# Kernel optimization log

Measured on AMD Instinct MI355X. Metric: run time of the kernel, lower is better.

Reference implementation:

```python
import jax, jax.numpy as jnp
import numpy as np

PS = 8          # patch_size
NF = 16         # n_feats
B, H, W = 4, 256, 256
C = NF * PS * PS          # channel_num = 1024
INNER = 3 * C             # heads * channel_num (no head split in source)
SCALE = C ** -0.5         # heads_feats = channel_num
EPS = 1e-5


def _patch(x, shift):
    # reflect-pad then non-overlapping unfold (kernel=PS, stride=PS)
    s = PS // 4
    p = shift * s
    x = jnp.pad(x, ((0, 0), (0, 0), (p, PS - p), (p, PS - p)), mode='reflect')
    b, c, hp, wp = x.shape
    x = x.reshape(b, c, hp // PS, PS, wp // PS, PS)
    # F.unfold ordering: (c, kh, kw) flattened per patch, patches row-major
    x = x.transpose(0, 2, 4, 1, 3, 5).reshape(b, (hp // PS) * (wp // PS), c * PS * PS)
    return x  # [B, N, C*PS*PS]


def _unpatch(x, h, w):
    # inverse of non-overlapping unfold, then crop right/bottom by PS
    b, n, d = x.shape
    c = d // (PS * PS)
    nh, nw = (h + PS) // PS, (w + PS) // PS
    x = x.reshape(b, nh, nw, c, PS, PS).transpose(0, 3, 1, 4, 2, 5)
    x = x.reshape(b, c, nh * PS, nw * PS)
    return x[:, :, :h, :w]


def _ln(x, g, b):
    m = x.mean(-1, keepdims=True)
    v = ((x - m) ** 2).mean(-1, keepdims=True)
    return (x - m) / jnp.sqrt(v + EPS) * g + b


def setup_inputs():
    key = jax.random.key(0)
    ks = jax.random.split(key, 16)
    w = lambda k, shp: jax.random.normal(k, shp, jnp.float32) * 0.02
    return {
        'dr_img': jax.random.normal(ks[0], (B, NF, H, W), jnp.float32),
        'dr_ref': jax.random.normal(ks[1], (B, NF, H, W), jnp.float32),
        'cl_ref': jax.random.normal(ks[2], (B, NF, H, W), jnp.float32),
        'ln_g': jnp.ones((C,), jnp.float32), 'ln_b': jnp.zeros((C,), jnp.float32),
        'Wq': w(ks[3], (C, INNER)), 'bq': jnp.zeros((INNER,), jnp.float32),
        'Wk': w(ks[4], (C, INNER)), 'bk': jnp.zeros((INNER,), jnp.float32),
        'Wv': w(ks[5], (C, INNER)), 'bv': jnp.zeros((INNER,), jnp.float32),
        'Wo': w(ks[6], (INNER, C)), 'bo': jnp.zeros((C,), jnp.float32),
        'ff_ln_g': jnp.ones((C,), jnp.float32), 'ff_ln_b': jnp.zeros((C,), jnp.float32),
        'W1': w(ks[7], (C, C)), 'b1': jnp.zeros((C,), jnp.float32),
        'W2': w(ks[8], (C, C)), 'b2': jnp.zeros((C,), jnp.float32),
    }


def reference(dr_img, dr_ref, cl_ref, ln_g, ln_b, Wq, bq, Wk, bk, Wv, bv,
              Wo, bo, ff_ln_g, ff_ln_b, W1, b1, W2, b2):
    def attn(q, k, v):
        qp = _ln(q, ln_g, ln_b) @ Wq + bq          # [B,N,3C]
        kp = _ln(k, ln_g, ln_b) @ Wk + bk
        vp = _ln(v, ln_g, ln_b) @ Wv + bv
        a = jax.nn.softmax(jnp.einsum('bnd,bmd->bnm', qp, kp) * SCALE, axis=-1)
        return jnp.einsum('bnm,bmd->bnd', a, vp) @ Wo + bo

    def ff(x):
        h = _ln(x, ff_ln_g, ff_ln_b)
        return jax.nn.gelu(h @ W1 + b1, approximate=False) @ W2 + b2

    x = _patch(dr_img, 0)                           # [B,N,C]
    for shift in range(4):
        k = jax.lax.stop_gradient(_patch(dr_ref, shift))
        v = jax.lax.stop_gradient(_patch(cl_ref, shift))
        x = attn(x, k, v) + x
        x = ff(x) + x
    return _unpatch(x, H, W)
```

## Files before the change

### kernel.cpp

```cpp
#include <hip/hip_runtime.h>

typedef unsigned short u16;
typedef float f32x4 __attribute__((ext_vector_type(4)));
typedef __bf16 bf16v8 __attribute__((ext_vector_type(8)));
typedef u16 u16x4 __attribute__((ext_vector_type(4)));

#define WAITV(n) asm volatile("s_waitcnt vmcnt(" #n ")" ::: "memory")
#define BAR() asm volatile("s_barrier" ::: "memory")
#define LGKM0() do { asm volatile("s_waitcnt lgkmcnt(0)" ::: "memory"); \
                     __builtin_amdgcn_sched_barrier(0); } while (0)

__device__ __forceinline__ u16 f2bf(float f) {
  union { float f; unsigned int u; } v; v.f = f;
  unsigned int x = v.u;
  x += 0x7fffu + ((x >> 16) & 1u);
  return (u16)(x >> 16);
}

__device__ __forceinline__ int refl(int i, int n) {
  i = (i < 0) ? -i : i;
  return (i >= n) ? (2 * n - 2 - i) : i;
}

__device__ __forceinline__ void gload_lds16(const void* g, void* l) {
  __builtin_amdgcn_global_load_lds(
      (const __attribute__((address_space(1))) void*)g,
      (__attribute__((address_space(3))) void*)l, 16, 0, 0);
}

enum { EPI_BF16_BIAS = 0, EPI_F32 = 1, EPI_BF16 = 2, EPI_F32_RES = 3, EPI_GELU = 4,
       EPI_BF16_BIASROW = 5 };

__device__ __forceinline__ void xcd_remap(int& bx, int& by, int& bz) {
  const int gx = gridDim.x, gy = gridDim.y;
  const int nwg = gx * gy * (int)gridDim.z;
  const int orig = ((int)blockIdx.z * gy + (int)blockIdx.y) * gx + (int)blockIdx.x;
  const int q = nwg >> 3, r = nwg & 7;
  const int xcd = orig & 7, loc = orig >> 3;
  const int swz = (xcd < r ? xcd * (q + 1) : r * (q + 1) + (xcd - r) * q) + loc;
  const int gxy = gx * gy;
  bz = swz / gxy;
  const int rem = swz - bz * gxy;
  by = rem / gx; bx = rem - by * gx;
}

template <int EPI>
__global__ __launch_bounds__(512, 2) void gemm256(
    const u16* __restrict__ A, const u16* __restrict__ Bt, void* __restrict__ Cp,
    const float* __restrict__ bias, int K, int Nld, long sA, long sB, long sC, long sBias)
{
  extern __shared__ __align__(16) u16 smem[];

  const int t = threadIdx.x;
  int bx, by, bz; xcd_remap(bx, by, bz);
  const int m0 = by * 256, n0 = bx * 256;

  const long Kb = (long)K * 2;
  const int sr8 = t >> 3;
  const int schunk = ((t & 7) ^ (sr8 & 7)) * 16;
  const char* Ag = (const char*)(A + (long)bz * sA + (long)m0 * K) + (long)sr8 * Kb + schunk;
  const char* Bg = (const char*)(Bt + (long)bz * sB + (long)n0 * K) + (long)sr8 * Kb + schunk;

  auto SA = [&](int d, int kt, int i0, int i1) {
    const long ko = (long)kt * 128;
    gload_lds16(Ag + (long)i0 * 64 * Kb + ko, &smem[d * 32768 + i0 * 4096 + t * 8]);
    gload_lds16(Ag + (long)i1 * 64 * Kb + ko, &smem[d * 32768 + i1 * 4096 + t * 8]);
  };
  auto SB = [&](int d, int kt, int i0, int i1) {
    const long ko = (long)kt * 128;
    gload_lds16(Bg + (long)i0 * 64 * Kb + ko, &smem[d * 32768 + 16384 + i0 * 4096 + t * 8]);
    gload_lds16(Bg + (long)i1 * 64 * Kb + ko, &smem[d * 32768 + 16384 + i1 * 4096 + t * 8]);
  };

  const int w = t >> 6, lane = t & 63;
  const int wm = (w >> 2) * 128, wn = (w & 3) * 64;
  const int lr = lane & 15, hi = lane >> 4;
  const int rc0 = ((0 * 4 + hi) ^ (lr & 7)) * 8;
  const int rc1 = ((1 * 4 + hi) ^ (lr & 7)) * 8;

  f32x4 acc[8][4];
  const f32x4 vzero = {0.f, 0.f, 0.f, 0.f};
#pragma unroll
  for (int i = 0; i < 8; i++)
#pragma unroll
    for (int j = 0; j < 4; j++) acc[i][j] = vzero;

  const int NT = K >> 6, NI = NT >> 1;

  SA(0, 0, 0, 1); SA(0, 0, 2, 3); SB(0, 0, 0, 1); SB(0, 0, 2, 3);
  SB(1, 1, 0, 2); SB(1, 1, 1, 3); SA(1, 1, 0, 2);
  WAITV(6);
  BAR();

  for (int i = 0; i < NI; i++) {
    const int t0 = 2 * i;
    const bool last = (i == NI - 1);
#pragma unroll
    for (int h = 0; h < 2; h++) {
      const u16* Ad = &smem[h * 32768];
      const u16* Bd = Ad + 16384;
      bf16v8 b8[4][2];
#pragma unroll
      for (int q = 0; q < 4; q++) {
        bf16v8 a8[2][2];
#pragma unroll
        for (int j = 0; j < 2; j++) {
          const int rbase = (wm + (2 * q + j) * 16 + lr) * 64;
          a8[j][0] = *(const bf16v8*)&Ad[rbase + rc0];
          a8[j][1] = *(const bf16v8*)&Ad[rbase + rc1];
        }
        if (q == 0) {
#pragma unroll
          for (int ni = 0; ni < 4; ni++) {
            const int rbase = (wn + ni * 16 + lr) * 64;
            b8[ni][0] = *(const bf16v8*)&Bd[rbase + rc0];
            b8[ni][1] = *(const bf16v8*)&Bd[rbase + rc1];
          }
        }
        if (h == 0) {
          if (q == 0)           SA(1, t0 + 1, 1, 3);
          else if (!last) {
            if (q == 1)         SB(0, t0 + 2, 0, 2);
            else if (q == 2)    SB(0, t0 + 2, 1, 3);
            else                SA(0, t0 + 2, 0, 2);
          }
        } else if (!last) {
          if (q == 0)           SA(0, t0 + 2, 1, 3);
          else if (q == 1)      SB(1, t0 + 3, 0, 2);
          else if (q == 2)      SB(1, t0 + 3, 1, 3);
          else                  SA(1, t0 + 3, 0, 2);
        }
        BAR();
        LGKM0();
        __builtin_amdgcn_s_setprio(1);
#pragma unroll
        for (int j = 0; j < 2; j++)
#pragma unroll
          for (int ni = 0; ni < 4; ni++) {
            acc[2 * q + j][ni] = __builtin_amdgcn_mfma_f32_16x16x32_bf16(a8[j][0], b8[ni][0], acc[2 * q + j][ni], 0, 0, 0);
            acc[2 * q + j][ni] = __builtin_amdgcn_mfma_f32_16x16x32_bf16(a8[j][1], b8[ni][1], acc[2 * q + j][ni], 0, 0, 0);
          }
        __builtin_amdgcn_s_setprio(0);
        if (h == 0 && q == 3) { if (last) { WAITV(0); } else { WAITV(6); } }
        if (h == 1 && q == 3 && !last) { WAITV(6); }
        BAR();
      }
    }
  }

#pragma unroll
  for (int mi = 0; mi < 8; mi++) {
    const int r0 = m0 + wm + mi * 16 + hi * 4;
#pragma unroll
    for (int ni = 0; ni < 4; ni++) {
      const int col = n0 + wn + ni * 16 + lr;
      float bvv = 0.f;
      if constexpr (EPI == EPI_BF16_BIAS) bvv = bias[bz * sBias + col];
#pragma unroll
      for (int j = 0; j < 4; j++) {
        const long idx = (long)(r0 + j) * Nld + col;
        float val = acc[mi][ni][j] + bvv;
        if constexpr (EPI == EPI_BF16_BIASROW) val += bias[r0 + j];
        if constexpr (EPI == EPI_BF16_BIAS || EPI == EPI_BF16 || EPI == EPI_BF16_BIASROW) {
          ((u16*)Cp + (long)bz * sC)[idx] = f2bf(val);
        } else {
          ((float*)Cp + (long)bz * sC)[idx] = val;
        }
      }
    }
  }
}

template <int EPI>
__global__ __launch_bounds__(256, 2) void gemm128(
    const u16* __restrict__ A, const u16* __restrict__ Bt, void* __restrict__ Cp,
    const float* __restrict__ bias, int K, int ldb, int Nld, long sA, long sB, long sC)
{
  extern __shared__ __align__(16) u16 smem[];
  u16* As = smem;
  u16* Bs = smem + 16384;

  const int t = threadIdx.x;
  int bx, by, bz; xcd_remap(bx, by, bz);
  const int m0 = by * 128, n0 = bx * 128;

  const long Ka = (long)K * 2;
  const long Kbb = (long)ldb * 2;
  const int sc = ((t & 7) * 16) ^ (((t >> 3) & 7) << 4);
  const char* Ag = (const char*)(A + (long)bz * sA + (long)m0 * K) + (long)(t >> 3) * Ka + sc;
  const char* Bg = (const char*)(Bt + (long)bz * sB + (long)n0 * ldb) + (long)(t >> 3) * Kbb + sc;

  auto STAGE = [&](int d, int kt) {
    const long ko = (long)kt * 128;
#pragma unroll
    for (int i = 0; i < 4; i++)
      gload_lds16(Ag + (long)i * 32 * Ka + ko, &As[d * 8192 + i * 2048 + t * 8]);
#pragma unroll
    for (int i = 0; i < 4; i++)
      gload_lds16(Bg + (long)i * 32 * Kbb + ko, &Bs[d * 8192 + i * 2048 + t * 8]);
  };

  const int w = t >> 6, lane = t & 63;
  const int wm = (w >> 1) * 64, wn = (w & 1) * 64;
  const int lr = lane & 15, hi = lane >> 4;
  const int cx = (lr & 7) << 4;

  f32x4 acc[4][4];
  const f32x4 vzero = {0.f, 0.f, 0.f, 0.f};
#pragma unroll
  for (int i = 0; i < 4; i++)
#pragma unroll
    for (int j = 0; j < 4; j++) acc[i][j] = vzero;

  const int NT = K >> 6;
  STAGE(0, 0);
  STAGE(1, 1);

  for (int kt = 0; kt < NT; kt++) {
    const int d = kt & 1;
    if (kt + 1 < NT) { WAITV(8); } else { WAITV(0); }
    BAR();

    const u16* Ad = &As[d * 8192];
    const u16* Bd = &Bs[d * 8192];
#pragma unroll
    for (int ks = 0; ks < 2; ks++) {
      bf16v8 a8[4], b8[4];
      const int cb = ks * 64;
#pragma unroll
      for (int mi = 0; mi < 4; mi++)
        a8[mi] = *(const bf16v8*)&Ad[(wm + mi * 16 + lr) * 64 + (((cb + hi * 16) ^ cx) >> 1)];
#pragma unroll
      for (int ni = 0; ni < 4; ni++)
        b8[ni] = *(const bf16v8*)&Bd[(wn + ni * 16 + lr) * 64 + (((cb + hi * 16) ^ cx) >> 1)];
      __builtin_amdgcn_s_setprio(1);
#pragma unroll
      for (int mi = 0; mi < 4; mi++)
#pragma unroll
        for (int ni = 0; ni < 4; ni++)
          acc[mi][ni] = __builtin_amdgcn_mfma_f32_16x16x32_bf16(a8[mi], b8[ni], acc[mi][ni], 0, 0, 0);
      __builtin_amdgcn_s_setprio(0);
    }
    asm volatile("s_waitcnt lgkmcnt(0)\n\ts_barrier" ::: "memory");
    if (kt + 2 < NT) STAGE(d, kt + 2);
  }

#pragma unroll
  for (int mi = 0; mi < 4; mi++) {
    const int r0 = m0 + wm + mi * 16 + hi * 4;
#pragma unroll
    for (int ni = 0; ni < 4; ni++) {
      const int col = n0 + wn + ni * 16 + lr;
      float bvv = 0.f;
      if constexpr (EPI == EPI_F32_RES || EPI == EPI_GELU) bvv = bias[col];
#pragma unroll
      for (int j = 0; j < 4; j++) {
        const long idx = (long)(r0 + j) * Nld + col;
        const float val = acc[mi][ni][j] + bvv;
        if constexpr (EPI == EPI_F32) {
          ((float*)Cp + (long)bz * sC)[idx] = val;
        } else if constexpr (EPI == EPI_F32_RES) {
          ((float*)Cp + (long)bz * sC)[idx] += val;
        } else if constexpr (EPI == EPI_GELU) {
          const float gv = 0.5f * val * (1.f + erff(val * 0.70710678118654752440f));
          ((u16*)Cp + (long)bz * sC)[idx] = f2bf(gv);
        } else {
          ((u16*)Cp + (long)bz * sC)[idx] = f2bf(val);
        }
      }
    }
  }
}

__global__ __launch_bounds__(256) void ln_kernel(const float* __restrict__ X,
    const float* __restrict__ g, const float* __restrict__ be, u16* __restrict__ Y)
{
  const long row = blockIdx.x;
  const int t = threadIdx.x;
  const float* xr = X + row * 1024;
  f32x4 v = *(const f32x4*)&xr[t * 4];
  float s = v[0] + v[1] + v[2] + v[3];
  float q = v[0]*v[0] + v[1]*v[1] + v[2]*v[2] + v[3]*v[3];
#pragma unroll
  for (int off = 32; off; off >>= 1) { s += __shfl_xor(s, off); q += __shfl_xor(q, off); }
  __shared__ float red[8];
  if ((t & 63) == 0) { red[t >> 6] = s; red[4 + (t >> 6)] = q; }
  __syncthreads();
  s = red[0] + red[1] + red[2] + red[3];
  q = red[4] + red[5] + red[6] + red[7];
  const float mean = s * (1.f / 1024.f);
  const float rstd = rsqrtf(q * (1.f / 1024.f) - mean * mean + 1e-5f);
  f32x4 gv = *(const f32x4*)&g[t * 4];
  f32x4 bv = *(const f32x4*)&be[t * 4];
  u16x4 o;
#pragma unroll
  for (int i = 0; i < 4; i++) o[i] = f2bf((v[i] - mean) * rstd * gv[i] + bv[i]);
  *(u16x4*)&Y[row * 1024 + t * 4] = o;
}

__global__ __launch_bounds__(256) void patch_kernel(const float* __restrict__ img,
    float* __restrict__ X, int shift)
{
  const int n = blockIdx.x, b = blockIdx.y, t = threadIdx.x;
  float* xr = X + ((long)b * 1152 + n) * 1024;
  if (n >= 1089) {
    const f32x4 z = {0.f, 0.f, 0.f, 0.f};
    *(f32x4*)&xr[t * 4] = z;
    return;
  }
  const int p = shift * 2;
  const int ph = n / 33, pw = n - ph * 33;
  const int d0 = t * 4;
  const int c = d0 >> 6, kh = (d0 >> 3) & 7, kw0 = d0 & 7;
  const int hh = refl(ph * 8 + kh - p, 256);
  const float* src = img + ((long)(b * 16 + c) * 256 + hh) * 256;
  f32x4 v;
#pragma unroll
  for (int i = 0; i < 4; i++) v[i] = src[refl(pw * 8 + kw0 + i - p, 256)];
  *(f32x4*)&xr[d0] = v;
}

__global__ __launch_bounds__(256) void patch_ln_kernel(const float* __restrict__ img,
    const float* __restrict__ g, const float* __restrict__ be, u16* __restrict__ Y, int shift)
{
  const int n = blockIdx.x, b = blockIdx.y, t = threadIdx.x;
  u16* yr = Y + ((long)b * 1152 + n) * 1024;
  if (n >= 1089) {
    const u16x4 z = {0, 0, 0, 0};
    *(u16x4*)&yr[t * 4] = z;
    return;
  }
  const int p = shift * 2;
  const int ph = n / 33, pw = n - ph * 33;
  const int d0 = t * 4;
  const int c = d0 >> 6, kh = (d0 >> 3) & 7, kw0 = d0 & 7;
  const int hh = refl(ph * 8 + kh - p, 256);
  const float* src = img + ((long)(b * 16 + c) * 256 + hh) * 256;
  float v[4];
#pragma unroll
  for (int i = 0; i < 4; i++) v[i] = src[refl(pw * 8 + kw0 + i - p, 256)];
  float s = v[0] + v[1] + v[2] + v[3];
  float q = v[0]*v[0] + v[1]*v[1] + v[2]*v[2] + v[3]*v[3];
#pragma unroll
  for (int off = 32; off; off >>= 1) { s += __shfl_xor(s, off); q += __shfl_xor(q, off); }
  __shared__ float red[8];
  if ((t & 63) == 0) { red[t >> 6] = s; red[4 + (t >> 6)] = q; }
  __syncthreads();
  s = red[0] + red[1] + red[2] + red[3];
  q = red[4] + red[5] + red[6] + red[7];
  const float mean = s * (1.f / 1024.f);
  const float rstd = rsqrtf(q * (1.f / 1024.f) - mean * mean + 1e-5f);
  u16x4 o;
#pragma unroll
  for (int i = 0; i < 4; i++) o[i] = f2bf((v[i] - mean) * rstd * g[d0 + i] + be[d0 + i]);
  *(u16x4*)&yr[d0] = o;
}

__global__ __launch_bounds__(256) void softmax_kernel(const float* __restrict__ L,
    u16* __restrict__ P)
{
  const int r = blockIdx.x, b = blockIdx.y, t = threadIdx.x;
  const float* Lr = L + ((long)b * 1152 + r) * 1152;
  u16* Pr = P + ((long)b * 1152 + r) * 1152;
  float v[5];
  float mx = -1e30f;
#pragma unroll
  for (int i = 0; i < 5; i++) {
    const int j = t + i * 256;
    v[i] = (j < 1089) ? Lr[j] * 0.03125f : -1e30f;
    mx = fmaxf(mx, v[i]);
  }
#pragma unroll
  for (int off = 32; off; off >>= 1) mx = fmaxf(mx, __shfl_xor(mx, off));
  __shared__ float sm[4];
  if ((t & 63) == 0) sm[t >> 6] = mx;
  __syncthreads();
  mx = fmaxf(fmaxf(sm[0], sm[1]), fmaxf(sm[2], sm[3]));
  float p[5];
  float s = 0.f;
#pragma unroll
  for (int i = 0; i < 5; i++) {
    const int j = t + i * 256;
    p[i] = (j < 1089) ? __expf(v[i] - mx) : 0.f;
    s += p[i];
  }
#pragma unroll
  for (int off = 32; off; off >>= 1) s += __shfl_xor(s, off);
  __shared__ float ss[4];
  if ((t & 63) == 0) ss[t >> 6] = s;
  __syncthreads();
  const float inv = 1.f / (ss[0] + ss[1] + ss[2] + ss[3]);
#pragma unroll
  for (int i = 0; i < 5; i++) {
    const int j = t + i * 256;
    if (j < 1152) Pr[j] = f2bf(p[i] * inv);
  }
}

__global__ __launch_bounds__(256) void wtrans_kernel(const float* __restrict__ W,
    u16* __restrict__ Wt, int K, int N)
{
  __shared__ float tile[32][33];
  const int n0 = blockIdx.x * 32, k0 = blockIdx.y * 32;
  const int tx = threadIdx.x & 31, ty = threadIdx.x >> 5;
#pragma unroll
  for (int i = 0; i < 4; i++)
    tile[ty + 8 * i][tx] = W[(long)(k0 + ty + 8 * i) * N + n0 + tx];
  __syncthreads();
#pragma unroll
  for (int i = 0; i < 4; i++)
    Wt[(long)(n0 + ty + 8 * i) * K + k0 + tx] = f2bf(tile[tx][ty + 8 * i]);
}

__global__ __launch_bounds__(256) void catbias_kernel(const float* __restrict__ a,
    const float* __restrict__ b, const float* __restrict__ c, float* __restrict__ o)
{
  const int i = blockIdx.x * 256 + threadIdx.x;
  o[i] = a[i]; o[3072 + i] = b[i]; o[6144 + i] = c[i];
}

__global__ __launch_bounds__(256) void unpatch_kernel(const float* __restrict__ X,
    float* __restrict__ out)
{
  const int idx = blockIdx.x * 256 + threadIdx.x;
  const int w = (idx & 63) * 4;
  const int h = (idx >> 6) & 255;
  const int c = (idx >> 14) & 15;
  const int b = idx >> 18;
  const int ph = h >> 3, kh = h & 7, pw = w >> 3, kw = w & 7;
  const long row = (long)b * 1152 + ph * 33 + pw;
  const int d = c * 64 + kh * 8 + kw;
  const f32x4 v = *(const f32x4*)&X[row * 1024 + d];
  *(f32x4*)&out[((long)(b * 16 + c) * 256 + h) * 256 + w] = v;
}

extern "C" void kernel_launch(void* const* d_in, const int* in_sizes, int n_in,
                              void* d_out, int out_size, void* d_ws, size_t ws_size,
                              hipStream_t stream)
{
  (void)in_sizes; (void)n_in; (void)out_size; (void)ws_size;
  const float* dr_img = (const float*)d_in[0];
  const float* dr_ref = (const float*)d_in[1];
  const float* cl_ref = (const float*)d_in[2];
  const float* ln_g = (const float*)d_in[3];
  const float* ln_be = (const float*)d_in[4];
  const float* Wq = (const float*)d_in[5];
  const float* bq = (const float*)d_in[6];
  const float* Wk = (const float*)d_in[7];
  const float* bk = (const float*)d_in[8];
  const float* Wv = (const float*)d_in[9];
  const float* bv = (const float*)d_in[10];
  const float* Wo = (const float*)d_in[11];
  const float* bo = (const float*)d_in[12];
  const float* ffg = (const float*)d_in[13];
  const float* ffb = (const float*)d_in[14];
  const float* W1 = (const float*)d_in[15];
  const float* b1 = (const float*)d_in[16];
  const float* W2 = (const float*)d_in[17];
  const float* b2 = (const float*)d_in[18];

  const long R = 1152;
  const long MR = 4 * R;

  char* ws = (char*)d_ws;
  size_t off = 0;
  auto alloc = [&](size_t bytes) -> void* {
    void* pp = ws + off;
    off += (bytes + 255) & ~(size_t)255;
    return pp;
  };
  float* x    = (float*)alloc((size_t)MR * 1024 * 4);
  u16* xkv_ln = (u16*)alloc((size_t)3 * MR * 1024 * 2);
  u16* qkv    = (u16*)alloc((size_t)3 * MR * 3072 * 2);
  float* lgt  = (float*)alloc((size_t)4 * R * R * 4);
  u16* P      = (u16*)alloc((size_t)4 * R * R * 2);
  u16* Wqkv_t = (u16*)alloc((size_t)3 * 3072 * 1024 * 2);
  u16* Wo_t   = (u16*)alloc((size_t)1024 * 3072 * 2);
  u16* W1_t   = (u16*)alloc((size_t)1024 * 1024 * 2);
  u16* W2_t   = (u16*)alloc((size_t)1024 * 1024 * 2);
  float* bcat = (float*)alloc((size_t)3 * 3072 * 4);

  u16* x_ln = xkv_ln;
  u16* v_ln = xkv_ln + (size_t)2 * MR * 1024;
  u16* h    = xkv_ln + (size_t)MR * 1024;
  u16* qp   = qkv;
  u16* kp   = qkv + (size_t)MR * 3072;
  u16* vT   = qkv + (size_t)2 * MR * 3072;
  u16* Wv_t = Wqkv_t + (size_t)2 * 3072 * 1024;

  wtrans_kernel<<<dim3(96, 32), 256, 0, stream>>>(Wq, Wqkv_t, 1024, 3072);
  wtrans_kernel<<<dim3(96, 32), 256, 0, stream>>>(Wk, Wqkv_t + (size_t)3072 * 1024, 1024, 3072);
  wtrans_kernel<<<dim3(96, 32), 256, 0, stream>>>(Wv, Wv_t, 1024, 3072);
  wtrans_kernel<<<dim3(32, 96), 256, 0, stream>>>(Wo, Wo_t, 3072, 1024);
  wtrans_kernel<<<dim3(32, 32), 256, 0, stream>>>(W1, W1_t, 1024, 1024);
  wtrans_kernel<<<dim3(32, 32), 256, 0, stream>>>(W2, W2_t, 1024, 1024);
  catbias_kernel<<<12, 256, 0, stream>>>(bq, bk, bv, bcat);

  patch_kernel<<<dim3(1152, 4), 256, 0, stream>>>(dr_img, x, 0);

  const long sAp = (long)MR * 1024;
  const long sBp = (long)3072 * 1024;
  const long sCp = (long)MR * 3072;
  const long sQb = R * 3072;
  const long sLb = R * R;

  for (int shift = 0; shift < 4; shift++) {
    ln_kernel<<<(int)MR, 256, 0, stream>>>(x, ln_g, ln_be, x_ln);
    patch_ln_kernel<<<dim3(1152, 4), 256, 0, stream>>>(dr_ref, ln_g, ln_be, xkv_ln + sAp, shift);
    patch_ln_kernel<<<dim3(1152, 4), 256, 0, stream>>>(cl_ref, ln_g, ln_be, v_ln, shift);

    gemm256<EPI_BF16_BIAS><<<dim3(12, 18, 2), 512, 131072, stream>>>(
        xkv_ln, Wqkv_t, qkv, bcat, 1024, 3072, sAp, sBp, sCp, 3072);

    gemm256<EPI_BF16_BIASROW><<<dim3(18, 12, 1), 512, 131072, stream>>>(
        Wv_t, v_ln, vT, bv, 1024, (int)MR, 0, 0, 0, 0);

    gemm128<EPI_F32><<<dim3(9, 9, 4), 256, 65536, stream>>>(
        qp, kp, lgt, nullptr, 3072, 3072, 1152, sQb, sQb, sLb);

    softmax_kernel<<<dim3(1152, 4), 256, 0, stream>>>(lgt, P);

    gemm128<EPI_BF16><<<dim3(24, 9, 4), 256, 65536, stream>>>(
        P, vT, qp, nullptr, 1152, (int)MR, 3072, sLb, R, sQb);

    gemm128<EPI_F32_RES><<<dim3(8, 36, 1), 256, 65536, stream>>>(
        qp, Wo_t, x, bo, 3072, 3072, 1024, 0, 0, 0);

    ln_kernel<<<(int)MR, 256, 0, stream>>>(x, ffg, ffb, x_ln);
    gemm128<EPI_GELU><<<dim3(8, 36, 1), 256, 65536, stream>>>(
        x_ln, W1_t, h, b1, 1024, 1024, 1024, 0, 0, 0);
    gemm128<EPI_F32_RES><<<dim3(8, 36, 1), 256, 65536, stream>>>(
        h, W2_t, x, b2, 1024, 1024, 1024, 0, 0, 0);
  }

  unpatch_kernel<<<4096, 256, 0, stream>>>(x, (float*)d_out);
}
```

Before: 1.408 ms.

## Run 128x128 GEMM tile with 8 waves instead of 4

```diff
diff --git a/kernel.cpp b/kernel.cpp
--- a/kernel.cpp
+++ b/kernel.cpp
@@ -172,45 +172,43 @@
 }
 
 template <int EPI>
-__global__ __launch_bounds__(256, 2) void gemm128(
+__global__ __launch_bounds__(512, 4) void gemm128(
     const u16* __restrict__ A, const u16* __restrict__ Bt, void* __restrict__ Cp,
     const float* __restrict__ bias, int K, int ldb, int Nld, long sA, long sB, long sC)
 {
   extern __shared__ __align__(16) u16 smem[];
-  u16* As = smem;
-  u16* Bs = smem + 16384;
 
   const int t = threadIdx.x;
   int bx, by, bz; xcd_remap(bx, by, bz);
   const int m0 = by * 128, n0 = bx * 128;
 
   const long Ka = (long)K * 2;
-  const long Kbb = (long)ldb * 2;
-  const int sc = ((t & 7) * 16) ^ (((t >> 3) & 7) << 4);
-  const char* Ag = (const char*)(A + (long)bz * sA + (long)m0 * K) + (long)(t >> 3) * Ka + sc;
-  const char* Bg = (const char*)(Bt + (long)bz * sB + (long)n0 * ldb) + (long)(t >> 3) * Kbb + sc;
+  const long Kb2 = (long)ldb * 2;
+  const int sr8 = t >> 3;
+  const int schunk = ((t & 7) ^ (sr8 & 7)) * 16;
+  const char* Ag = (const char*)(A + (long)bz * sA + (long)m0 * K) + (long)sr8 * Ka + schunk;
+  const char* Bg = (const char*)(Bt + (long)bz * sB + (long)n0 * ldb) + (long)sr8 * Kb2 + schunk;
 
   auto STAGE = [&](int d, int kt) {
     const long ko = (long)kt * 128;
-#pragma unroll
-    for (int i = 0; i < 4; i++)
-      gload_lds16(Ag + (long)i * 32 * Ka + ko, &As[d * 8192 + i * 2048 + t * 8]);
-#pragma unroll
-    for (int i = 0; i < 4; i++)
-      gload_lds16(Bg + (long)i * 32 * Kbb + ko, &Bs[d * 8192 + i * 2048 + t * 8]);
+    gload_lds16(Ag + ko,                &smem[d * 16384 + t * 8]);
+    gload_lds16(Ag + 64 * Ka + ko,      &smem[d * 16384 + 4096 + t * 8]);
+    gload_lds16(Bg + ko,                &smem[d * 16384 + 8192 + t * 8]);
+    gload_lds16(Bg + 64 * Kb2 + ko,     &smem[d * 16384 + 12288 + t * 8]);
   };
 
   const int w = t >> 6, lane = t & 63;
-  const int wm = (w >> 1) * 64, wn = (w & 1) * 64;
+  const int wm = (w >> 2) * 64, wn = (w & 3) * 32;
   const int lr = lane & 15, hi = lane >> 4;
-  const int cx = (lr & 7) << 4;
-
-  f32x4 acc[4][4];
+  const int rc0 = ((0 * 4 + hi) ^ (lr & 7)) * 8;
+  const int rc1 = ((1 * 4 + hi) ^ (lr & 7)) * 8;
+
+  f32x4 acc[4][2];
   const f32x4 vzero = {0.f, 0.f, 0.f, 0.f};
 #pragma unroll
   for (int i = 0; i < 4; i++)
 #pragma unroll
-    for (int j = 0; j < 4; j++) acc[i][j] = vzero;
+    for (int j = 0; j < 2; j++) acc[i][j] = vzero;
 
   const int NT = K >> 6;
   STAGE(0, 0);
@@ -218,29 +216,33 @@
 
   for (int kt = 0; kt < NT; kt++) {
     const int d = kt & 1;
-    if (kt + 1 < NT) { WAITV(8); } else { WAITV(0); }
+    if (kt + 1 < NT) { WAITV(4); } else { WAITV(0); }
     BAR();
 
-    const u16* Ad = &As[d * 8192];
-    const u16* Bd = &Bs[d * 8192];
-#pragma unroll
-    for (int ks = 0; ks < 2; ks++) {
-      bf16v8 a8[4], b8[4];
-      const int cb = ks * 64;
-#pragma unroll
-      for (int mi = 0; mi < 4; mi++)
-        a8[mi] = *(const bf16v8*)&Ad[(wm + mi * 16 + lr) * 64 + (((cb + hi * 16) ^ cx) >> 1)];
-#pragma unroll
-      for (int ni = 0; ni < 4; ni++)
-        b8[ni] = *(const bf16v8*)&Bd[(wn + ni * 16 + lr) * 64 + (((cb + hi * 16) ^ cx) >> 1)];
-      __builtin_amdgcn_s_setprio(1);
-#pragma unroll
-      for (int mi = 0; mi < 4; mi++)
-#pragma unroll
-        for (int ni = 0; ni < 4; ni++)
-          acc[mi][ni] = __builtin_amdgcn_mfma_f32_16x16x32_bf16(a8[mi], b8[ni], acc[mi][ni], 0, 0, 0);
-      __builtin_amdgcn_s_setprio(0);
+    const u16* Ad = &smem[d * 16384];
+    const u16* Bd = Ad + 8192;
+    bf16v8 a8[4][2], b8[2][2];
+#pragma unroll
+    for (int mi = 0; mi < 4; mi++) {
+      const int rbase = (wm + mi * 16 + lr) * 64;
+      a8[mi][0] = *(const bf16v8*)&Ad[rbase + rc0];
+      a8[mi][1] = *(const bf16v8*)&Ad[rbase + rc1];
     }
+#pragma unroll
+    for (int ni = 0; ni < 2; ni++) {
+      const int rbase = (wn + ni * 16 + lr) * 64;
+      b8[ni][0] = *(const bf16v8*)&Bd[rbase + rc0];
+      b8[ni][1] = *(const bf16v8*)&Bd[rbase + rc1];
+    }
+    __builtin_amdgcn_s_setprio(1);
+#pragma unroll
+    for (int mi = 0; mi < 4; mi++)
+#pragma unroll
+      for (int ni = 0; ni < 2; ni++) {
+        acc[mi][ni] = __builtin_amdgcn_mfma_f32_16x16x32_bf16(a8[mi][0], b8[ni][0], acc[mi][ni], 0, 0, 0);
+        acc[mi][ni] = __builtin_amdgcn_mfma_f32_16x16x32_bf16(a8[mi][1], b8[ni][1], acc[mi][ni], 0, 0, 0);
+      }
+    __builtin_amdgcn_s_setprio(0);
     asm volatile("s_waitcnt lgkmcnt(0)\n\ts_barrier" ::: "memory");
     if (kt + 2 < NT) STAGE(d, kt + 2);
   }
@@ -249,7 +251,7 @@
   for (int mi = 0; mi < 4; mi++) {
     const int r0 = m0 + wm + mi * 16 + hi * 4;
 #pragma unroll
-    for (int ni = 0; ni < 4; ni++) {
+    for (int ni = 0; ni < 2; ni++) {
       const int col = n0 + wn + ni * 16 + lr;
       float bvv = 0.f;
       if constexpr (EPI == EPI_F32_RES || EPI == EPI_GELU) bvv = bias[col];
@@ -515,21 +517,21 @@
     gemm256<EPI_BF16_BIASROW><<<dim3(18, 12, 1), 512, 131072, stream>>>(
         Wv_t, v_ln, vT, bv, 1024, (int)MR, 0, 0, 0, 0);
 
-    gemm128<EPI_F32><<<dim3(9, 9, 4), 256, 65536, stream>>>(
+    gemm128<EPI_F32><<<dim3(9, 9, 4), 512, 65536, stream>>>(
         qp, kp, lgt, nullptr, 3072, 3072, 1152, sQb, sQb, sLb);
 
     softmax_kernel<<<dim3(1152, 4), 256, 0, stream>>>(lgt, P);
 
-    gemm128<EPI_BF16><<<dim3(24, 9, 4), 256, 65536, stream>>>(
+    gemm128<EPI_BF16><<<dim3(24, 9, 4), 512, 65536, stream>>>(
         P, vT, qp, nullptr, 1152, (int)MR, 3072, sLb, R, sQb);
 
-    gemm128<EPI_F32_RES><<<dim3(8, 36, 1), 256, 65536, stream>>>(
+    gemm128<EPI_F32_RES><<<dim3(8, 36, 1), 512, 65536, stream>>>(
         qp, Wo_t, x, bo, 3072, 3072, 1024, 0, 0, 0);
 
     ln_kernel<<<(int)MR, 256, 0, stream>>>(x, ffg, ffb, x_ln);
-    gemm128<EPI_GELU><<<dim3(8, 36, 1), 256, 65536, stream>>>(
+    gemm128<EPI_GELU><<<dim3(8, 36, 1), 512, 65536, stream>>>(
         x_ln, W1_t, h, b1, 1024, 1024, 1024, 0, 0, 0);
-    gemm128<EPI_F32_RES><<<dim3(8, 36, 1), 256, 65536, stream>>>(
+    gemm128<EPI_F32_RES><<<dim3(8, 36, 1), 512, 65536, stream>>>(
         h, W2_t, x, b2, 1024, 1024, 1024, 0, 0, 0);
   }
 
```

Result: faster. 1.334 ms (-5.3%).
